# Performance work log

Measured on AMD Instinct MI355X. Metric: run time of the kernel, lower is better.

The kernel has to match this reference:

```python
import jax, jax.numpy as jnp
import numpy as np

N_HEADS = 4
N_HIDDEN = 256  # out_features with concat=False
SLOPE = 0.1
NEG_INF = -9e15


def setup_inputs() -> dict:
    key = jax.random.key(0)
    k1, k2, k3, k4 = jax.random.split(key, 4)
    N, F_IN = 4096, 512
    h = jax.random.normal(k1, (N, F_IN), dtype=jnp.float32)
    adj_mat = jax.random.randint(k2, (N, N), 0, 2, dtype=jnp.int32)
    # xavier_normal gain=1.414
    W = jax.random.normal(k3, (F_IN, N_HIDDEN * N_HEADS), dtype=jnp.float32) * (
        1.414 * np.sqrt(2.0 / (F_IN + N_HIDDEN * N_HEADS)))
    a = jax.random.normal(k4, (N_HEADS, 2 * N_HIDDEN, 1), dtype=jnp.float32) * (
        1.414 * np.sqrt(2.0 / (2 * N_HIDDEN + 1)))
    return {"h": h, "adj_mat": adj_mat, "W": W, "a": a}


def reference(h, adj_mat, W, a):
    N = h.shape[0]
    # [N, H*D] -> [H, N, D]
    ht = (h @ W).reshape(N, N_HEADS, N_HIDDEN).transpose(1, 0, 2)
    lr = jax.nn.leaky_relu(ht, SLOPE)
    # additive attention: a split into source/target halves
    src = jnp.einsum('hnd,hd->hn', lr, a[:, :N_HIDDEN, 0])   # [H, N]
    tgt = jnp.einsum('hnd,hd->hn', lr, a[:, N_HIDDEN:, 0])   # [H, N]
    e = src[:, :, None] + tgt[:, None, :]                    # [H, N, N]
    e = jnp.where(adj_mat > 0, e, NEG_INF)
    attn = jax.nn.softmax(e, axis=-1)
    out = jnp.einsum('hnm,hmd->hnd', attn, ht)               # [H, N, D]
    return out.mean(axis=0)                                  # concat=False -> mean over heads
```

## Files before the change

### kernel.cpp

```cpp
#include <hip/hip_runtime.h>

#define N_NODES 4096
#define F_IN 512
#define NHID 256
#define HD 1024
#define NPAD 1152

typedef _Float16 half8 __attribute__((ext_vector_type(8)));
typedef _Float16 half4 __attribute__((ext_vector_type(4)));
typedef float floatx4 __attribute__((ext_vector_type(4)));
typedef float float4v __attribute__((ext_vector_type(4)));
typedef int int4v __attribute__((ext_vector_type(4)));
typedef unsigned int uint4v __attribute__((ext_vector_type(4)));

__device__ __forceinline__ float bf2f(unsigned short u) {
  union { unsigned int i; float f; } x; x.i = ((unsigned int)u) << 16; return x.f;
}

__device__ __forceinline__ void async_copy16(const void* g, void* l) {
  __builtin_amdgcn_global_load_lds((const __attribute__((address_space(1))) void*)g,
                                   (__attribute__((address_space(3))) void*)l, 16, 0, 0);
}

template <typename OutT>
__device__ __forceinline__ void gemm_core(
    const _Float16* __restrict__ A, const _Float16* __restrict__ BT,
    OutT* __restrict__ C, int K, int ldc, int klen, long csz,
    int lin, int nbx, int nby, int total,
    _Float16* __restrict__ sA, _Float16* __restrict__ sB)
{
  int tile = ((total & 7) == 0) ? ((lin & 7) * (total >> 3) + (lin >> 3)) : lin;
  const int n_idx = tile % nbx;
  const int rem   = tile / nbx;
  const int m_idx = rem % nby;
  const int kz    = rem / nby;

  const int n0 = n_idx * 128;
  const int m0 = m_idx * 128;
  const int kbeg = kz * klen;
  OutT* Cz = C + (long)kz * csz;

  const int t = threadIdx.x;
  const int w = t >> 6;
  const int lane = t & 63;
  const int wm = (w >> 1) << 6;
  const int wn = (w & 1) << 6;

  floatx4 acc[4][4] = {};

  const int l4 = lane >> 2;
  const int kk = (lane & 3) << 3;
  const int c0 = w << 1;

  const _Float16* gA = A + (long)m0 * K;
  const _Float16* gBT = BT + (long)n0 * K;

  const int koff = (lane >> 4) << 3;
  const int rA = wm + (lane & 15);
  const int rB = wn + (lane & 15);

  const int nt = klen >> 5;

  auto STAGE = [&](int buf, int k0) {
#pragma unroll
    for (int p = 0; p < 2; ++p) {
      const int c = c0 + p;
      const int row = c * 16 + l4;
      async_copy16(gA + (long)row * K + k0 + kk, &sA[buf * 4096 + c * 512 + lane * 8]);
      async_copy16(gBT + (long)row * K + k0 + kk, &sB[buf * 4096 + c * 512 + lane * 8]);
    }
  };

  STAGE(0, kbeg);
  if (nt > 1) STAGE(1, kbeg + 32);

  int cur = 0;
  for (int it = 0; it < nt; ++it) {
    const int k0 = kbeg + it * 32;

    if (it + 1 < nt) asm volatile("s_waitcnt vmcnt(4)" ::: "memory");
    else             asm volatile("s_waitcnt vmcnt(0)" ::: "memory");
    __builtin_amdgcn_s_barrier();

    half8 af[4], bf[4];
#pragma unroll
    for (int i = 0; i < 4; ++i)
      af[i] = *(const half8*)&sA[cur * 4096 + (rA + i * 16) * 32 + koff];
#pragma unroll
    for (int i = 0; i < 4; ++i)
      bf[i] = *(const half8*)&sB[cur * 4096 + (rB + i * 16) * 32 + koff];

    asm volatile("s_waitcnt lgkmcnt(0)" ::: "memory");
    __builtin_amdgcn_sched_barrier(0);

    const int nxt = (cur + 2 >= 3) ? cur - 1 : cur + 2;
    if (it + 2 < nt) STAGE(nxt, k0 + 64);

#pragma unroll
    for (int i = 0; i < 4; ++i)
#pragma unroll
      for (int j = 0; j < 4; ++j)
        acc[i][j] = __builtin_amdgcn_mfma_f32_16x16x32_f16(af[i], bf[j], acc[i][j], 0, 0, 0);

    cur = (cur + 1 >= 3) ? 0 : cur + 1;
  }

  const int q4 = (lane >> 4) << 2;
#pragma unroll
  for (int i = 0; i < 4; ++i) {
#pragma unroll
    for (int j = 0; j < 4; ++j) {
      const int gr = m0 + wm + i * 16 + q4;
      const int gc = n0 + wn + j * 16 + (lane & 15);
#pragma unroll
      for (int r = 0; r < 4; ++r)
        Cz[(long)(gr + r) * ldc + gc] = (OutT)acc[i][j][r];
    }
  }
}

template <typename OutT>
__global__ __launch_bounds__(256) void gemm_bt(
    const _Float16* __restrict__ A, const _Float16* __restrict__ BT,
    OutT* __restrict__ C, int K, int ldc, int klen, long csz)
{
  __shared__ _Float16 sA[3 * 128 * 32];
  __shared__ _Float16 sB[3 * 128 * 32];
  const int nbx = gridDim.x, nby = gridDim.y;
  const int total = nbx * nby * gridDim.z;
  const int lin = blockIdx.x + nbx * (blockIdx.y + nby * blockIdx.z);
  gemm_core<OutT>(A, BT, C, K, ldc, klen, csz, lin, nbx, nby, total, sA, sB);
}

__global__ __launch_bounds__(256) void prep_kernel(
    const void* __restrict__ h, _Float16* __restrict__ hF,
    const void* __restrict__ a, float* __restrict__ aF,
    const void* __restrict__ W, _Float16* __restrict__ WT,
    const int* __restrict__ adj, _Float16* __restrict__ adjF)
{
  const int t = threadIdx.x;
  const int b = blockIdx.x;

  if (b >= 1153) {
    const int i = (b - 1153) * 256 + t;
    int4v A = ((const int4v*)adj)[2 * i];
    int4v B = ((const int4v*)adj)[2 * i + 1];
    half8 o;
#pragma unroll
    for (int e = 0; e < 4; ++e) {
      o[e]     = (_Float16)(A[e] > 0 ? 1.0f : 0.0f);
      o[4 + e] = (_Float16)(B[e] > 0 ? 1.0f : 0.0f);
    }
    ((half8*)adjF)[i] = o;
    return;
  }

  __shared__ int red[256];
  __shared__ _Float16 tile[64][72];
  const unsigned short* hb = (const unsigned short*)h;
  int cnt = 0;
#pragma unroll
  for (int q = 0; q < 4; ++q) {
    int e = (hb[t * 4 + q] >> 7) & 0xFF;
    cnt += (e >= 115 && e <= 135) ? 1 : 0;
  }
  red[t] = cnt; __syncthreads();
  for (int s = 128; s > 0; s >>= 1) { if (t < s) red[t] += red[t + s]; __syncthreads(); }
  const int bf = (red[0] >= 900) ? 1 : 0;
  __syncthreads();

  if (b < 1024) {
    const int i = b * 256 + t;
    half8 o;
    if (bf) {
      union { uint4v v; unsigned short s[8]; } u;
      u.v = ((const uint4v*)h)[i];
#pragma unroll
      for (int e = 0; e < 8; ++e) o[e] = (_Float16)bf2f(u.s[e]);
    } else {
      const float4v* f = (const float4v*)h + 2 * i;
      float4v x0 = f[0], x1 = f[1];
#pragma unroll
      for (int e = 0; e < 4; ++e) { o[e] = (_Float16)x0[e]; o[4 + e] = (_Float16)x1[e]; }
    }
    ((half8*)hF)[i] = o;
  } else if (b == 1024) {
#pragma unroll
    for (int e = 0; e < 8; ++e) {
      int idx = t * 8 + e;
      aF[idx] = bf ? bf2f(((const unsigned short*)a)[idx]) : ((const float*)a)[idx];
    }
  } else {
    const int bb = b - 1025;
    const int k0 = (bb & 7) * 64, n0 = (bb >> 3) * 64;
    const int r = t >> 3, c = t & 7;
#pragma unroll
    for (int q = 0; q < 2; ++q) {
      int k = r + q * 32;
      half8 v;
      if (bf) {
        union { uint4v vv; unsigned short s[8]; } u;
        u.vv = *(const uint4v*)&((const unsigned short*)W)[(long)(k0 + k) * HD + n0 + c * 8];
#pragma unroll
        for (int e = 0; e < 8; ++e) v[e] = (_Float16)bf2f(u.s[e]);
      } else {
        const float4v* f = (const float4v*)&((const float*)W)[(long)(k0 + k) * HD + n0 + c * 8];
        float4v x0 = f[0], x1 = f[1];
#pragma unroll
        for (int e = 0; e < 4; ++e) { v[e] = (_Float16)x0[e]; v[4 + e] = (_Float16)x1[e]; }
      }
      *(half8*)&tile[k][c * 8] = v;
    }
    __syncthreads();
#pragma unroll
    for (int q = 0; q < 2; ++q) {
      int n = r + q * 32;
      half8 o;
#pragma unroll
      for (int e = 0; e < 8; ++e) o[e] = tile[c * 8 + e][n];
      *(half8*)&WT[(long)(n0 + n) * F_IN + k0 + c * 8] = o;
    }
  }
}

__global__ void tgt_kernel(const _Float16* __restrict__ ht, const float* __restrict__ aF,
                           float* __restrict__ tgt) {
  const int i = blockIdx.x;
  const int t = threadIdx.x, h = t >> 6, lane = t & 63;
  half4 v = *(const half4*)&ht[(long)i * HD + h * NHID + lane * 4];
  float4v av = *(const float4v*)&aF[h * 512 + NHID + lane * 4];
  float s = 0.f;
#pragma unroll
  for (int e = 0; e < 4; ++e) {
    float x = (float)v[e];
    x = x > 0.f ? x : 0.1f * x;
    s += x * av[e];
  }
#pragma unroll
  for (int o = 32; o > 0; o >>= 1) s += __shfl_down(s, o);
  if (lane == 0) tgt[h * N_NODES + i] = s;
}

__global__ void scaled_transpose_kernel(const _Float16* __restrict__ ht, const float* __restrict__ tgt,
                                        _Float16* __restrict__ VT) {
  __shared__ _Float16 tile[64][72];
  __shared__ float red[4];
  const int j0 = blockIdx.x * 64;
  const int t = threadIdx.x;
  const int w = t >> 6, lane = t & 63;

  if (blockIdx.y == 16) {
    const float* row = tgt + w * N_NODES;
    float m = -3.0e38f;
#pragma unroll
    for (int q = 0; q < 16; ++q) {
      float4v v = *(const float4v*)&row[(lane + q * 64) * 4];
#pragma unroll
      for (int e = 0; e < 4; ++e) m = fmaxf(m, v[e]);
    }
#pragma unroll
    for (int o = 32; o > 0; o >>= 1) m = fmaxf(m, __shfl_down(m, o));
    if (lane == 0) red[w] = m;
    __syncthreads();
    const float mh = red[w];
    const int j = j0 + lane;
    VT[(long)(HD + w) * N_NODES + j] = (_Float16)__expf(row[j] - mh);
    return;
  }

  const int n0 = blockIdx.y * 64;
  const int h = n0 >> 8;
  const float* row = tgt + h * N_NODES;
  const int r = t >> 3, c = t & 7;
#pragma unroll
  for (int q = 0; q < 2; ++q) {
    int j = r + q * 32;
    *(half8*)&tile[j][c * 8] = *(const half8*)&ht[(long)(j0 + j) * HD + n0 + c * 8];
  }
  float m = -3.0e38f;
#pragma unroll
  for (int q = 0; q < 4; ++q) {
    float4v v = *(const float4v*)&row[(t + q * 256) * 4];
#pragma unroll
    for (int e = 0; e < 4; ++e) m = fmaxf(m, v[e]);
  }
#pragma unroll
  for (int o = 32; o > 0; o >>= 1) m = fmaxf(m, __shfl_down(m, o));
  if (lane == 0) red[w] = m;
  __syncthreads();
  m = fmaxf(fmaxf(red[0], red[1]), fmaxf(red[2], red[3]));

  float w8[8];
#pragma unroll
  for (int e = 0; e < 8; ++e)
    w8[e] = __expf(row[j0 + c * 8 + e] - m);
#pragma unroll
  for (int q = 0; q < 2; ++q) {
    int n = r + q * 32;
    half8 o;
#pragma unroll
    for (int e = 0; e < 8; ++e) {
      int j = c * 8 + e;
      o[e] = (_Float16)(w8[e] * (float)tile[j][n]);
    }
    *(half8*)&VT[(long)(n0 + n) * N_NODES + j0 + c * 8] = o;
  }
}

__global__ void epilogue_kernel(const float* __restrict__ S, float* __restrict__ out, int ns) {
  const int i = blockIdx.x, d = threadIdx.x;
  const long SZ = (long)N_NODES * NPAD;
  float num[4] = {0.f, 0.f, 0.f, 0.f};
  float den[4] = {0.f, 0.f, 0.f, 0.f};
  for (int z = 0; z < ns; ++z) {
    const float* row = S + z * SZ + (long)i * NPAD;
#pragma unroll
    for (int h = 0; h < 4; ++h) {
      num[h] += row[h * NHID + d];
      den[h] += row[HD + h];
    }
  }
  float r = 0.f;
#pragma unroll
  for (int h = 0; h < 4; ++h) r += num[h] / den[h];
  out[(long)i * NHID + d] = 0.25f * r;
}

extern "C" void kernel_launch(void* const* d_in, const int* in_sizes, int n_in,
                              void* d_out, int out_size, void* d_ws, size_t ws_size,
                              hipStream_t stream) {
  const void* h = nullptr; const int* adj = nullptr; const void* W = nullptr; const void* a = nullptr;
  for (int i = 0; i < n_in; ++i) {
    switch (in_sizes[i]) {
      case 2097152:  h   = d_in[i]; break;
      case 16777216: adj = (const int*)d_in[i]; break;
      case 524288:   W   = d_in[i]; break;
      case 2048:     a   = d_in[i]; break;
      default: break;
    }
  }
  float* out = (float*)d_out;

  char* ws = (char*)d_ws;
  const size_t OFF_ADJF = 0;
  const size_t OFF_VT   = 33554432;
  const size_t OFF_TGT  = OFF_VT + 9437184;
  const size_t OFF_WBUF = OFF_TGT + 65536;
  const size_t OFF_M    = OFF_WBUF + 65536;
  const size_t OFF_AF   = OFF_M + 256;
  const size_t OFF_X    = OFF_AF + 8192;
  const size_t SPART    = 18874368;

  int ns = 1;
  if      (ws_size >= OFF_X + 2 * SPART) ns = 2;
  if (ws_size < OFF_X + SPART || !h || !adj || !W || !a) return;

  _Float16* adjF = (_Float16*)(ws + OFF_ADJF);
  _Float16* VT   = (_Float16*)(ws + OFF_VT);
  float*    tgt  = (float*)(ws + OFF_TGT);
  float*    aF   = (float*)(ws + OFF_AF);
  _Float16* hF = (_Float16*)(ws + OFF_X);
  _Float16* WT = (_Float16*)(ws + OFF_X + 4194304);
  _Float16* ht = (_Float16*)(ws + OFF_X + 5242880);
  float*    S  = (float*)(ws + OFF_X);

  prep_kernel<<<9345, 256, 0, stream>>>(h, hF, a, aF, W, WT, adj, adjF);
  gemm_bt<_Float16><<<dim3(8, 32, 1), 256, 0, stream>>>(hF, WT, ht, F_IN, HD, F_IN, 0);
  tgt_kernel<<<4096, 256, 0, stream>>>(ht, aF, tgt);
  scaled_transpose_kernel<<<dim3(64, 17), 256, 0, stream>>>(ht, tgt, VT);
  gemm_bt<float><<<dim3(9, 32, ns), 256, 0, stream>>>(adjF, VT, S, N_NODES, NPAD,
                                                      N_NODES / ns, (long)N_NODES * NPAD);
  epilogue_kernel<<<4096, 256, 0, stream>>>(S, out, ns);
}
```

Baseline: 185.7 us.

## Fuse adjacency int-to-fp16 conversion into the attention GEMM A-operand load

Removes the separate pass that converted the int32 adjacency matrix into a 32MB fp16 buffer, and instead has a new GEMM kernel async-copy int32 adjacency tiles into LDS and convert them in registers to fp16 0/1 values before the MFMA. This eliminates a full 64MB read plus 32MB write and reread of the intermediate. In exchange the GEMM streams twice as many bytes for A per tile, uses a larger LDS footprint (int tiles), and may have lower occupancy. The adjacency is re-read once per N-tile column (9 times), doubling that traffic relative to fp16.

```diff
diff --git a/kernel.cpp b/kernel.cpp
--- a/kernel.cpp
+++ b/kernel.cpp
@@ -132,29 +132,143 @@
   gemm_core<OutT>(A, BT, C, K, ldc, klen, csz, lin, nbx, nby, total, sA, sB);
 }
 
+__global__ __launch_bounds__(256) void gemm_adj_kernel(
+    const int* __restrict__ adj, const _Float16* __restrict__ BT, float* __restrict__ C,
+    int K, int ldc, int klen, long csz)
+{
+  __shared__ int      sAi[3 * 128 * 32];
+  __shared__ _Float16 sB [3 * 128 * 32];
+  const int nbx = gridDim.x, nby = gridDim.y;
+  const int total = nbx * nby * gridDim.z;
+  const int lin = blockIdx.x + nbx * (blockIdx.y + nby * blockIdx.z);
+
+  int tile = ((total & 7) == 0) ? ((lin & 7) * (total >> 3) + (lin >> 3)) : lin;
+  const int n_idx = tile % nbx;
+  const int rem   = tile / nbx;
+  const int m_idx = rem % nby;
+  const int kz    = rem / nby;
+
+  const int n0 = n_idx * 128;
+  const int m0 = m_idx * 128;
+  const int kbeg = kz * klen;
+  float* Cz = C + (long)kz * csz;
+
+  const int t = threadIdx.x;
+  const int w = t >> 6;
+  const int lane = t & 63;
+  const int wm = (w >> 1) << 6;
+  const int wn = (w & 1) << 6;
+
+  floatx4 acc[4][4] = {};
+
+  const int l4 = lane >> 2;
+  const int kkB = (lane & 3) << 3;
+  const int c0 = w << 1;
+  const _Float16* gBT = BT + (long)n0 * K;
+
+  const int* gAi = adj + (long)m0 * K;
+  const int arow  = t >> 3;
+  const int aslot = (t & 7) ^ ((t >> 3) & 7);
+
+  const int koff = (lane >> 4) << 3;
+  const int g2 = (lane >> 4) << 1;
+  const int rA = wm + (lane & 15);
+  const int rB = wn + (lane & 15);
+
+  const int nt = klen >> 5;
+
+  auto STAGE = [&](int buf, int k0) {
+#pragma unroll
+    for (int q = 0; q < 4; ++q) {
+      const int row = q * 32 + arow;
+      async_copy16(gAi + (long)row * K + k0 + aslot * 4,
+                   &sAi[buf * 4096 + (q * 256 + t) * 4]);
+    }
+#pragma unroll
+    for (int p = 0; p < 2; ++p) {
+      const int c = c0 + p;
+      const int row = c * 16 + l4;
+      async_copy16(gBT + (long)row * K + k0 + kkB, &sB[buf * 4096 + c * 512 + lane * 8]);
+    }
+  };
+
+  STAGE(0, kbeg);
+  if (nt > 1) STAGE(1, kbeg + 32);
+
+  int cur = 0;
+  for (int it = 0; it < nt; ++it) {
+    const int k0 = kbeg + it * 32;
+    if (it + 1 < nt) asm volatile("s_waitcnt vmcnt(6)" ::: "memory");
+    else             asm volatile("s_waitcnt vmcnt(0)" ::: "memory");
+    __builtin_amdgcn_s_barrier();
+
+    int4v a0[4], a1[4];
+    half8 bf[4];
+#pragma unroll
+    for (int i = 0; i < 4; ++i) {
+      const int r = rA + i * 16;
+      const int rm = r & 7;
+      a0[i] = *(const int4v*)&sAi[cur * 4096 + r * 32 + ((g2) ^ rm) * 4];
+      a1[i] = *(const int4v*)&sAi[cur * 4096 + r * 32 + ((g2 + 1) ^ rm) * 4];
+    }
+#pragma unroll
+    for (int j = 0; j < 4; ++j)
+      bf[j] = *(const half8*)&sB[cur * 4096 + (rB + j * 16) * 32 + koff];
+
+    asm volatile("s_waitcnt lgkmcnt(0)" ::: "memory");
+    __builtin_amdgcn_sched_barrier(0);
+
+    const int nxt = (cur + 2 >= 3) ? cur - 1 : cur + 2;
+    if (it + 2 < nt) STAGE(nxt, k0 + 64);
+
+    half8 af[4];
+#pragma unroll
+    for (int i = 0; i < 4; ++i) {
+      union { unsigned u[4]; half8 h; } pk;
+      unsigned x0 = (unsigned)a0[i][0], x1 = (unsigned)a0[i][1],
+               x2 = (unsigned)a0[i][2], x3 = (unsigned)a0[i][3],
+               y0 = (unsigned)a1[i][0], y1 = (unsigned)a1[i][1],
+               y2 = (unsigned)a1[i][2], y3 = (unsigned)a1[i][3];
+      x0 = x0 < 1u ? x0 : 1u; x1 = x1 < 1u ? x1 : 1u;
+      x2 = x2 < 1u ? x2 : 1u; x3 = x3 < 1u ? x3 : 1u;
+      y0 = y0 < 1u ? y0 : 1u; y1 = y1 < 1u ? y1 : 1u;
+      y2 = y2 < 1u ? y2 : 1u; y3 = y3 < 1u ? y3 : 1u;
+      pk.u[0] = (x0 + (x1 << 16)) * 0x3C00u;
+      pk.u[1] = (x2 + (x3 << 16)) * 0x3C00u;
+      pk.u[2] = (y0 + (y1 << 16)) * 0x3C00u;
+      pk.u[3] = (y2 + (y3 << 16)) * 0x3C00u;
+      af[i] = pk.h;
+    }
+
+#pragma unroll
+    for (int i = 0; i < 4; ++i)
+#pragma unroll
+      for (int j = 0; j < 4; ++j)
+        acc[i][j] = __builtin_amdgcn_mfma_f32_16x16x32_f16(af[i], bf[j], acc[i][j], 0, 0, 0);
+
+    cur = (cur + 1 >= 3) ? 0 : cur + 1;
+  }
+
+  const int q4 = (lane >> 4) << 2;
+#pragma unroll
+  for (int i = 0; i < 4; ++i) {
+#pragma unroll
+    for (int j = 0; j < 4; ++j) {
+      const int gr = m0 + wm + i * 16 + q4;
+      const int gc = n0 + wn + j * 16 + (lane & 15);
+#pragma unroll
+      for (int r = 0; r < 4; ++r)
+        Cz[(long)(gr + r) * ldc + gc] = acc[i][j][r];
+    }
+  }
+}
+
 __global__ __launch_bounds__(256) void prep_kernel(
     const void* __restrict__ h, _Float16* __restrict__ hF,
     const void* __restrict__ a, float* __restrict__ aF,
-    const void* __restrict__ W, _Float16* __restrict__ WT,
-    const int* __restrict__ adj, _Float16* __restrict__ adjF)
+    const void* __restrict__ W, _Float16* __restrict__ WT)
 {
   const int t = threadIdx.x;
-  const int b = blockIdx.x;
-
-  if (b >= 1153) {
-    const int i = (b - 1153) * 256 + t;
-    int4v A = ((const int4v*)adj)[2 * i];
-    int4v B = ((const int4v*)adj)[2 * i + 1];
-    half8 o;
-#pragma unroll
-    for (int e = 0; e < 4; ++e) {
-      o[e]     = (_Float16)(A[e] > 0 ? 1.0f : 0.0f);
-      o[4 + e] = (_Float16)(B[e] > 0 ? 1.0f : 0.0f);
-    }
-    ((half8*)adjF)[i] = o;
-    return;
-  }
-
   __shared__ int red[256];
   __shared__ _Float16 tile[64][72];
   const unsigned short* hb = (const unsigned short*)h;
@@ -169,6 +283,7 @@
   const int bf = (red[0] >= 900) ? 1 : 0;
   __syncthreads();
 
+  const int b = blockIdx.x;
   if (b < 1024) {
     const int i = b * 256 + t;
     half8 o;
@@ -342,8 +457,7 @@
   float* out = (float*)d_out;
 
   char* ws = (char*)d_ws;
-  const size_t OFF_ADJF = 0;
-  const size_t OFF_VT   = 33554432;
+  const size_t OFF_VT   = 0;
   const size_t OFF_TGT  = OFF_VT + 9437184;
   const size_t OFF_WBUF = OFF_TGT + 65536;
   const size_t OFF_M    = OFF_WBUF + 65536;
@@ -355,7 +469,6 @@
   if      (ws_size >= OFF_X + 2 * SPART) ns = 2;
   if (ws_size < OFF_X + SPART || !h || !adj || !W || !a) return;
 
-  _Float16* adjF = (_Float16*)(ws + OFF_ADJF);
   _Float16* VT   = (_Float16*)(ws + OFF_VT);
   float*    tgt  = (float*)(ws + OFF_TGT);
   float*    aF   = (float*)(ws + OFF_AF);
@@ -364,11 +477,11 @@
   _Float16* ht = (_Float16*)(ws + OFF_X + 5242880);
   float*    S  = (float*)(ws + OFF_X);
 
-  prep_kernel<<<9345, 256, 0, stream>>>(h, hF, a, aF, W, WT, adj, adjF);
+  prep_kernel<<<1153, 256, 0, stream>>>(h, hF, a, aF, W, WT);
   gemm_bt<_Float16><<<dim3(8, 32, 1), 256, 0, stream>>>(hF, WT, ht, F_IN, HD, F_IN, 0);
   tgt_kernel<<<4096, 256, 0, stream>>>(ht, aF, tgt);
   scaled_transpose_kernel<<<dim3(64, 17), 256, 0, stream>>>(ht, tgt, VT);
-  gemm_bt<float><<<dim3(9, 32, ns), 256, 0, stream>>>(adjF, VT, S, N_NODES, NPAD,
-                                                      N_NODES / ns, (long)N_NODES * NPAD);
+  gemm_adj_kernel<<<dim3(9, 32, ns), 256, 0, stream>>>(adj, VT, S, N_NODES, NPAD,
+                                                       N_NODES / ns, (long)N_NODES * NPAD);
   epilogue_kernel<<<4096, 256, 0, stream>>>(S, out, ns);
 }
```

Result: slower. 223.7 us (+20.5%).
